# Optimization experiments

Measured on AMD Instinct MI355X. Metric: run time of the kernel, lower is better.

The kernel has to match this reference:

```python
import jax, jax.numpy as jnp
import numpy as np

NUM_EXPERTS = 8
TOP_K = 2
HIDDEN = 2048
INTER = 5632
NUM_TOKENS = 8192


def setup_inputs() -> dict:
    key = jax.random.key(0)
    ks = jax.random.split(key, 5)
    s_h = 1.0 / np.sqrt(HIDDEN)
    s_i = 1.0 / np.sqrt(INTER)
    return {
        "hidden_states": jax.random.normal(ks[0], (NUM_TOKENS, HIDDEN), jnp.float32),
        # router: ReplicatedLinear(hidden, num_experts, bias=False) -> weight [E, H]
        "w_router": jax.random.normal(ks[1], (NUM_EXPERTS, HIDDEN), jnp.float32) * s_h,
        # FusedMoE SiLU-gated MLP per expert: gate/up [E, H, I], down [E, I, H]
        "w_gate": jax.random.normal(ks[2], (NUM_EXPERTS, HIDDEN, INTER), jnp.float32) * s_h,
        "w_up": jax.random.normal(ks[3], (NUM_EXPERTS, HIDDEN, INTER), jnp.float32) * s_h,
        "w_down": jax.random.normal(ks[4], (NUM_EXPERTS, INTER, HIDDEN), jnp.float32) * s_i,
    }


def reference(hidden_states, w_router, w_gate, w_up, w_down):
    x = hidden_states  # [T, H]
    # Router linear (no bias)
    router_logits = x @ w_router.T  # [T, E]
    # FusedMoE topk: softmax over all experts, take top-k, renormalize=False
    probs = jax.nn.softmax(router_logits.astype(jnp.float32), axis=-1)
    topk_w, topk_idx = jax.lax.top_k(probs, TOP_K)  # [T, k]
    topk_w = topk_w.astype(x.dtype)

    out = jnp.zeros_like(x)
    for e in range(NUM_EXPERTS):
        # combine weight for tokens that routed to expert e (0 otherwise)
        w_e = jnp.sum(jnp.where(topk_idx == e, topk_w, 0.0), axis=-1)  # [T]
        h = jax.nn.silu(x @ w_gate[e]) * (x @ w_up[e])  # [T, I]
        out = out + (h @ w_down[e]) * w_e[:, None]
    return out
```

## Files before the change

### kernel.cpp

```cpp
#include <hip/hip_runtime.h>
#include <hip/hip_bf16.h>
#include <cstdint>

#define NTOK 8192
#define NEXP 8
#define HID  2048
#define INTR 5632
#define NT1  44
#define NT2  16

#define TCNT_OFF    4096u
#define SLOT_OFF    65536u
#define T2S_OFF     262144u
#define W2_OFF      393216u
#define LISTS_OFF   524288u
#define WL_OFF      786432u
#define WG_OFF      2097152u
#define WBYTES      184549376u
#define WU_OFF      (WG_OFF + WBYTES)
#define HF_OFF      (WU_OFF + WBYTES)
#define HFBYTES     207618048u
#define XG_OFF      (HF_OFF + HFBYTES)

typedef float f32x4  __attribute__((ext_vector_type(4)));
typedef short s16x8  __attribute__((ext_vector_type(8)));
typedef short s16x4  __attribute__((ext_vector_type(4)));

__device__ __forceinline__ short bfc(float f) {
  __hip_bfloat16 h = __float2bfloat16(f);
  return __builtin_bit_cast(short, h);
}
__device__ __forceinline__ float b2f(short s) {
  unsigned u = ((unsigned)(unsigned short)s) << 16;
  return __builtin_bit_cast(float, u);
}
__device__ __forceinline__ s16x8 pk8(float4 a, float4 b) {
  s16x8 v;
  v[0]=bfc(a.x); v[1]=bfc(a.y); v[2]=bfc(a.z); v[3]=bfc(a.w);
  v[4]=bfc(b.x); v[5]=bfc(b.y); v[6]=bfc(b.z); v[7]=bfc(b.w);
  return v;
}
__device__ __forceinline__ void gload16(const void* g, void* l) {
  __builtin_amdgcn_global_load_lds((const __attribute__((address_space(1))) void*)g,
                                   (__attribute__((address_space(3))) void*)l, 16, 0, 0);
}

#define DSR128(dst, addr, IMM) \
  asm volatile("ds_read_b128 %0, %1 offset:" IMM : "=v"(dst) : "v"(addr))
#define WAITLGKM(N) do { \
  asm volatile("s_waitcnt lgkmcnt(" #N ")" ::: "memory"); \
  __builtin_amdgcn_sched_barrier(0); } while (0)
#define WAITVM(N) do { \
  asm volatile("s_waitcnt vmcnt(" #N ")" ::: "memory"); \
  __builtin_amdgcn_sched_barrier(0); } while (0)

#define MFMA_BF16 __builtin_amdgcn_mfma_f32_16x16x32_bf16

__global__ __launch_bounds__(256, 4) void prep_kernel(
    const float* __restrict__ src, short* __restrict__ dst,
    int KT, int NP, int Nsrc) {
  __shared__ float tile[32 * 132];
  const int b = blockIdx.x;
  const int np = b % NP;
  const int kt = (b / NP) % KT;
  const int e  = b / (NP * KT);
  const int tid = threadIdx.x;
  const float* s = src + (size_t)e * KT * 32 * (size_t)Nsrc + (size_t)kt * 32 * Nsrc + np * 128;
#pragma unroll
  for (int i = 0; i < 4; i++) {
    const int idx = tid + i * 256;
    const int row = idx >> 5, c4 = idx & 31;
    float4 v = *(const float4*)(s + (size_t)row * Nsrc + c4 * 4);
    *(float4*)(tile + row * 132 + c4 * 4) = v;
  }
  __syncthreads();
  short* dbase = dst + ((size_t)(e * KT + kt) * (NP * 8) + np * 8) * 512;
#pragma unroll
  for (int i = 0; i < 2; i++) {
    const int c = tid + i * 256;
    const int lane = c & 63;
    const int nf = c >> 6;
    const int n = nf * 16 + (lane & 15);
    const int kb = (lane >> 4) * 8;
    s16x8 o;
#pragma unroll
    for (int j = 0; j < 8; j++) o[j] = bfc(tile[(kb + j) * 132 + n]);
    *(s16x8*)(dbase + (size_t)c * 8) = o;
  }
}

__global__ void router_kernel(const float* __restrict__ x, const float* __restrict__ wr,
                              int* __restrict__ cnt, int* __restrict__ lists,
                              float* __restrict__ wlists) {
  const int wave = threadIdx.x >> 6;
  const int lane = threadIdx.x & 63;
  const int t = blockIdx.x * 4 + wave;
  if (t >= NTOK) return;
  float acc[NEXP];
#pragma unroll
  for (int e = 0; e < NEXP; e++) acc[e] = 0.f;
  const float* xrow = x + (size_t)t * HID;
#pragma unroll
  for (int j = 0; j < HID / 256; j++) {
    const int k = j * 256 + lane * 4;
    float4 xv = *(const float4*)(xrow + k);
#pragma unroll
    for (int e = 0; e < NEXP; e++) {
      float4 wv = *(const float4*)(wr + e * HID + k);
      acc[e] += xv.x * wv.x + xv.y * wv.y + xv.z * wv.z + xv.w * wv.w;
    }
  }
#pragma unroll
  for (int e = 0; e < NEXP; e++) {
    float v = acc[e];
    for (int off = 32; off; off >>= 1) v += __shfl_xor(v, off, 64);
    acc[e] = v;
  }
  if (lane == 0) {
    float m = acc[0];
#pragma unroll
    for (int e = 1; e < NEXP; e++) m = fmaxf(m, acc[e]);
    float p[NEXP], s = 0.f;
#pragma unroll
    for (int e = 0; e < NEXP; e++) { p[e] = __expf(acc[e] - m); s += p[e]; }
    const float inv = 1.f / s;
    int e1 = 0; float b1 = p[0];
#pragma unroll
    for (int e = 1; e < NEXP; e++) if (p[e] > b1) { b1 = p[e]; e1 = e; }
    int e2 = -1; float b2 = -1.f;
#pragma unroll
    for (int e = 0; e < NEXP; e++) if (e != e1 && p[e] > b2) { b2 = p[e]; e2 = e; }
    const int pos1 = atomicAdd(&cnt[e1], 1);
    lists[e1 * NTOK + pos1] = t; wlists[e1 * NTOK + pos1] = b1 * inv;
    const int pos2 = atomicAdd(&cnt[e2], 1);
    lists[e2 * NTOK + pos2] = t; wlists[e2 * NTOK + pos2] = b2 * inv;
  }
}

__global__ void offsets_kernel(const int* __restrict__ cnt, int* __restrict__ poffs) {
  if (threadIdx.x == 0 && blockIdx.x == 0) {
    int o = 0;
#pragma unroll
    for (int e = 0; e < NEXP; e++) { poffs[e] = o; o += ((cnt[e] + 255) >> 8) << 8; }
    poffs[NEXP] = o;
  }
}

__global__ void slotmap_kernel(const int* __restrict__ cnt, const int* __restrict__ poffs,
                               const int* __restrict__ lists, const float* __restrict__ wlists,
                               int* __restrict__ slotlist, int* __restrict__ tcnt,
                               int* __restrict__ tok2slot, float* __restrict__ w2) {
  const int e = blockIdx.x;
  const int c = cnt[e], base = poffs[e];
  for (int pos = threadIdx.x; pos < c; pos += blockDim.x) {
    const int tok = lists[e * NTOK + pos];
    const int slot = base + pos;
    slotlist[slot] = tok;
    const int j = atomicAdd(&tcnt[tok], 1);
    tok2slot[tok * 2 + j] = slot;
    w2[tok * 2 + j] = wlists[e * NTOK + pos];
  }
}

__global__ __launch_bounds__(256, 4) void gather_kernel(
    const float* __restrict__ x, const int* __restrict__ slotlist,
    short* __restrict__ xg) {
  const int c = blockIdx.x * 256 + threadIdx.x;
  const int cl = c & 63;
  const int fragid = c >> 6;
  const int f = fragid & 15;
  const int kt = (fragid >> 4) & 63;
  const int gmt = fragid >> 10;
  const int tok = slotlist[gmt * 256 + f * 16 + (cl & 15)];
  const float* s = x + (size_t)tok * HID + kt * 32 + (cl >> 4) * 8;
  float4 a = *(const float4*)s, b = *(const float4*)(s + 4);
  *(s16x8*)(xg + (size_t)c * 8) = pk8(a, b);
}

__global__ __launch_bounds__(512, 1) void gemm1_kernel(
    const short* __restrict__ xg, const short* __restrict__ wgb,
    const short* __restrict__ wub, const int* __restrict__ cnt,
    const int* __restrict__ poffs, short* __restrict__ hfrag) {
  const int P = blockIdx.x;
  const int xcd = P & 7, slot = P >> 3;
  const int mt = slot & 31, jj = slot >> 5;
  const int g = jj * 8 + xcd;
  const int e = g / NT1, nt = g % NT1;
  if (mt * 256 >= cnt[e]) return;
  const int gmt = (poffs[e] >> 8) + mt;
  const int tid = threadIdx.x;
  const int w = tid >> 6, lane = tid & 63;
  const int wm = w >> 1, wn = w & 1;

  __shared__ __align__(16) short Lds[3 * 16384];
  const uint32_t ldsbase = (uint32_t)(uintptr_t)&Lds[0];

  const short* srcA  = xg  + (size_t)gmt * 64 * 16 * 512 + tid * 8;
  const short* srcBg = wgb + (((size_t)e * 64) * 352 + nt * 8) * 512 + tid * 8;
  const short* srcBu = wub + (((size_t)e * 64) * 352 + nt * 8) * 512 + tid * 8;

  const uint32_t roA = wm * 4096 + lane * 16;
  const uint32_t roB = 16384 + wn * 4096 + lane * 16;
  const uint32_t roU = 24576 + wn * 4096 + lane * 16;

  f32x4 accG[4][4], accU[4][4];
#pragma unroll
  for (int i = 0; i < 4; i++)
#pragma unroll
    for (int j = 0; j < 4; j++) {
      accG[i][j] = f32x4{0.f, 0.f, 0.f, 0.f};
      accU[i][j] = f32x4{0.f, 0.f, 0.f, 0.f};
    }

#define STG1(WB) do {                                                           \
    short* d = (short*)Lds + ((WB) >> 1);                                       \
    gload16(srcA,          d + w * 512);                                        \
    gload16(srcA + 4096,   d + 4096 + w * 512);                                 \
    gload16(srcBg,         d + 8192 + w * 512);                                 \
    gload16(srcBu,         d + 12288 + w * 512);                                \
    srcA += 8192; srcBg += 180224; srcBu += 180224; } while (0)

#define MMQ(NF)                                                                 \
  { __builtin_amdgcn_s_setprio(1);                                              \
    accG[0][NF] = MFMA_BF16(af[0], bg[NF], accG[0][NF], 0, 0, 0);               \
    accU[0][NF] = MFMA_BF16(af[0], bu[NF], accU[0][NF], 0, 0, 0);               \
    accG[1][NF] = MFMA_BF16(af[1], bg[NF], accG[1][NF], 0, 0, 0);               \
    accU[1][NF] = MFMA_BF16(af[1], bu[NF], accU[1][NF], 0, 0, 0);               \
    accG[2][NF] = MFMA_BF16(af[2], bg[NF], accG[2][NF], 0, 0, 0);               \
    accU[2][NF] = MFMA_BF16(af[2], bu[NF], accU[2][NF], 0, 0, 0);               \
    accG[3][NF] = MFMA_BF16(af[3], bg[NF], accG[3][NF], 0, 0, 0);               \
    accU[3][NF] = MFMA_BF16(af[3], bu[NF], accU[3][NF], 0, 0, 0);               \
    __builtin_amdgcn_s_setprio(0); }

#define G1_BODY(RB, WB, VMN, DOSTG)                                             \
  {                                                                             \
    WAITVM(VMN);                                                                \
    __builtin_amdgcn_s_barrier();                                               \
    const uint32_t rb = ldsbase + (RB);                                         \
    s16x8 af[4], bg[4], bu[4];                                                  \
    DSR128(bg[0], rb + roB, "0");    DSR128(bu[0], rb + roU, "0");              \
    DSR128(af[0], rb + roA, "0");    DSR128(af[1], rb + roA, "1024");           \
    DSR128(af[2], rb + roA, "2048"); DSR128(af[3], rb + roA, "3072");           \
    DSR128(bg[1], rb + roB, "1024"); DSR128(bu[1], rb + roU, "1024");           \
    DSR128(bg[2], rb + roB, "2048"); DSR128(bu[2], rb + roU, "2048");           \
    DSR128(bg[3], rb + roB, "3072"); DSR128(bu[3], rb + roU, "3072");           \
    if (DOSTG) { STG1(WB); }                                                    \
    WAITLGKM(6);                                                                \
    MMQ(0)                                                                      \
    WAITLGKM(4);                                                                \
    MMQ(1)                                                                      \
    WAITLGKM(2);                                                                \
    MMQ(2)                                                                      \
    WAITLGKM(0);                                                                \
    MMQ(3)                                                                      \
  }

  STG1(0);
  STG1(32768);
  for (int it = 0; it < 20; ++it) {
    G1_BODY(0,     65536, 4, 1)
    G1_BODY(32768, 0,     4, 1)
    G1_BODY(65536, 32768, 4, 1)
  }
  G1_BODY(0,     65536, 4, 1)
  G1_BODY(32768, 0,     4, 1)
  G1_BODY(65536, 0,     4, 0)
  G1_BODY(0,     0,     0, 0)
#undef G1_BODY
#undef MMQ
#undef STG1

  short* tr = (short*)Lds;
  __syncthreads();
#pragma unroll
  for (int mf = 0; mf < 4; mf++)
#pragma unroll
    for (int reg = 0; reg < 4; reg++) {
      const int row = wm * 64 + mf * 16 + (lane >> 4) * 4 + reg;
#pragma unroll
      for (int nf = 0; nf < 4; nf++) {
        const int col = wn * 64 + nf * 16 + (lane & 15);
        const float gv = accG[mf][nf][reg];
        const float uv = accU[mf][nf][reg];
        tr[row * 136 + col] = bfc((gv / (1.f + __expf(-gv))) * uv);
      }
    }
  __syncthreads();
  short* hb = hfrag + (((size_t)gmt * 176 + nt * 4) * 16) * 512;
#pragma unroll
  for (int i = 0; i < 8; i++) {
    const int c = tid + i * 512;
    const int cl = c & 63;
    const int f = (c >> 6) & 15;
    const int ktl = c >> 10;
    const int rr = f * 16 + (cl & 15);
    s16x8 v = *(const s16x8*)(tr + rr * 136 + ktl * 32 + (cl >> 4) * 8);
    *(s16x8*)(hb + ((size_t)ktl * 16 + f) * 512 + cl * 8) = v;
  }
}

__global__ __launch_bounds__(512, 4) void gemm2_kernel(
    const short* __restrict__ hfrag, const short* __restrict__ wdb,
    const int* __restrict__ cnt, const int* __restrict__ poffs,
    __hip_bfloat16* __restrict__ pout) {
  const int P = blockIdx.x;
  const int xcd = P & 7, r = P >> 3;
  const int nt = r & 15, emq = r >> 4;
  const int gm = emq * 8 + xcd;
  const int e = gm >> 5, mt = gm & 31;
  if (mt * 256 >= cnt[e]) return;
  const int gmt = (poffs[e] >> 8) + mt;
  const int n0 = nt * 128;
  const int tid = threadIdx.x;
  const int w = tid >> 6, lane = tid & 63;
  const int wm = w >> 1, wn = w & 1;

  __shared__ __align__(16) short Lds[3 * 12288];
  const uint32_t ldsbase = (uint32_t)(uintptr_t)&Lds[0];

  const short* srcA = hfrag + (size_t)gmt * 176 * 16 * 512 + tid * 8;
  const short* srcB = wdb + (((size_t)e * 176) * 128 + nt * 8) * 512 + tid * 8;

  const uint32_t roA = wm * 4096 + lane * 16;
  const uint32_t roB = 16384 + wn * 4096 + lane * 16;

  f32x4 acc[4][4];
#pragma unroll
  for (int i = 0; i < 4; i++)
#pragma unroll
    for (int j = 0; j < 4; j++) acc[i][j] = f32x4{0.f, 0.f, 0.f, 0.f};

#define STG2(WB) do {                                                           \
    short* d = (short*)Lds + ((WB) >> 1);                                       \
    gload16(srcA,        d + w * 512);                                          \
    gload16(srcA + 4096, d + 4096 + w * 512);                                   \
    gload16(srcB,        d + 8192 + w * 512);                                   \
    srcA += 8192; srcB += 65536; } while (0)

#define MMQ2(NF)                                                                \
  { __builtin_amdgcn_s_setprio(1);                                              \
    acc[0][NF] = MFMA_BF16(af[0], bf[NF], acc[0][NF], 0, 0, 0);                 \
    acc[1][NF] = MFMA_BF16(af[1], bf[NF], acc[1][NF], 0, 0, 0);                 \
    acc[2][NF] = MFMA_BF16(af[2], bf[NF], acc[2][NF], 0, 0, 0);                 \
    acc[3][NF] = MFMA_BF16(af[3], bf[NF], acc[3][NF], 0, 0, 0);                 \
    __builtin_amdgcn_s_setprio(0); }

#define G2_BODY(RB, WB, VMN, DOSTG)                                             \
  {                                                                             \
    WAITVM(VMN);                                                                \
    __builtin_amdgcn_s_barrier();                                               \
    const uint32_t rb = ldsbase + (RB);                                         \
    s16x8 af[4], bf[4];                                                         \
    DSR128(bf[0], rb + roB, "0");                                               \
    DSR128(af[0], rb + roA, "0");    DSR128(af[1], rb + roA, "1024");           \
    DSR128(af[2], rb + roA, "2048"); DSR128(af[3], rb + roA, "3072");           \
    DSR128(bf[1], rb + roB, "1024");                                            \
    DSR128(bf[2], rb + roB, "2048");                                            \
    DSR128(bf[3], rb + roB, "3072");                                            \
    if (DOSTG) { STG2(WB); }                                                    \
    WAITLGKM(3);                                                                \
    MMQ2(0)                                                                     \
    WAITLGKM(2);                                                                \
    MMQ2(1)                                                                     \
    WAITLGKM(1);                                                                \
    MMQ2(2)                                                                     \
    WAITLGKM(0);                                                                \
    MMQ2(3)                                                                     \
  }

  STG2(0);
  STG2(24576);
  for (int it = 0; it < 58; ++it) {
    G2_BODY(0,     49152, 3, 1)
    G2_BODY(24576, 0,     3, 1)
    G2_BODY(49152, 24576, 3, 1)
  }
  G2_BODY(0,     0, 3, 0)
  G2_BODY(24576, 0, 0, 0)
#undef G2_BODY
#undef MMQ2
#undef STG2

  const int slotb = poffs[e] + mt * 256;
#pragma unroll
  for (int mf = 0; mf < 4; mf++) {
#pragma unroll
    for (int reg = 0; reg < 4; reg++) {
      const int row = wm * 64 + mf * 16 + (lane >> 4) * 4 + reg;
      __hip_bfloat16* op = pout + (size_t)(slotb + row) * HID + n0 + wn * 64 + (lane & 15);
#pragma unroll
      for (int nf = 0; nf < 4; nf++)
        op[nf * 16] = __float2bfloat16(acc[mf][nf][reg]);
    }
  }
}

__global__ __launch_bounds__(256, 8) void combine_kernel(
    const __hip_bfloat16* __restrict__ pout, const int* __restrict__ tok2slot,
    const float* __restrict__ w2, float* __restrict__ out) {
  const int t = blockIdx.x;
  const int s0 = tok2slot[2 * t], s1 = tok2slot[2 * t + 1];
  const float w0 = w2[2 * t], w1 = w2[2 * t + 1];
  const short* p0 = (const short*)pout + (size_t)s0 * HID;
  const short* p1 = (const short*)pout + (size_t)s1 * HID;
  float* o = out + (size_t)t * HID;
  const int i = threadIdx.x;
  s16x8 a = *(const s16x8*)(p0 + i * 8);
  s16x8 b = *(const s16x8*)(p1 + i * 8);
  float4 r0, r1;
  r0.x = w0 * b2f(a[0]) + w1 * b2f(b[0]);
  r0.y = w0 * b2f(a[1]) + w1 * b2f(b[1]);
  r0.z = w0 * b2f(a[2]) + w1 * b2f(b[2]);
  r0.w = w0 * b2f(a[3]) + w1 * b2f(b[3]);
  r1.x = w0 * b2f(a[4]) + w1 * b2f(b[4]);
  r1.y = w0 * b2f(a[5]) + w1 * b2f(b[5]);
  r1.z = w0 * b2f(a[6]) + w1 * b2f(b[6]);
  r1.w = w0 * b2f(a[7]) + w1 * b2f(b[7]);
  *(float4*)(o + i * 8) = r0;
  *(float4*)(o + i * 8 + 4) = r1;
}

extern "C" void kernel_launch(void* const* d_in, const int* in_sizes, int n_in,
                              void* d_out, int out_size, void* d_ws, size_t ws_size,
                              hipStream_t stream) {
  const float* x  = (const float*)d_in[0];
  const float* wr = (const float*)d_in[1];
  const float* wg = (const float*)d_in[2];
  const float* wu = (const float*)d_in[3];
  const float* wd = (const float*)d_in[4];
  float* out = (float*)d_out;
  char* ws = (char*)d_ws;

  int* cnt      = (int*)ws;
  int* poffs    = (int*)(ws + 64);
  int* tcnt     = (int*)(ws + TCNT_OFF);
  int* slotlist = (int*)(ws + SLOT_OFF);
  int* tok2slot = (int*)(ws + T2S_OFF);
  float* w2     = (float*)(ws + W2_OFF);
  int* lists    = (int*)(ws + LISTS_OFF);
  float* wlists = (float*)(ws + WL_OFF);
  short* wgb    = (short*)(ws + WG_OFF);
  short* wub    = (short*)(ws + WU_OFF);
  short* wdb    = (short*)(ws + WG_OFF);
  short* hfrag  = (short*)(ws + HF_OFF);
  short* xg     = (short*)(ws + XG_OFF);
  __hip_bfloat16* pout = (__hip_bfloat16*)(ws + XG_OFF);

  hipMemsetAsync(ws, 0, 256, stream);
  hipMemsetAsync(ws + TCNT_OFF, 0, 32768, stream);
  hipMemsetAsync(ws + SLOT_OFF, 0, 73728, stream);

  router_kernel<<<NTOK / 4, 256, 0, stream>>>(x, wr, cnt, lists, wlists);
  offsets_kernel<<<1, 64, 0, stream>>>(cnt, poffs);
  slotmap_kernel<<<NEXP, 256, 0, stream>>>(cnt, poffs, lists, wlists, slotlist, tcnt, tok2slot, w2);
  gather_kernel<<<18432, 256, 0, stream>>>(x, slotlist, xg);
  prep_kernel<<<NEXP * 64 * 44, 256, 0, stream>>>(wg, wgb, 64, 44, INTR);
  prep_kernel<<<NEXP * 64 * 44, 256, 0, stream>>>(wu, wub, 64, 44, INTR);
  gemm1_kernel<<<8 * 32 * NT1, 512, 0, stream>>>(xg, wgb, wub, cnt, poffs, hfrag);
  prep_kernel<<<NEXP * 176 * 16, 256, 0, stream>>>(wd, wdb, 176, 16, HID);
  gemm2_kernel<<<8 * 16 * 32, 512, 0, stream>>>(hfrag, wdb, cnt, poffs, pout);
  combine_kernel<<<NTOK, 256, 0, stream>>>(pout, tok2slot, w2, out);
}
```

Measured before the change: 1.670 ms.

## Load gemm1 A fragments straight to registers and double-buffer B through LDS

In gemm1, the A (token) fragments are now loaded from global memory directly into registers with inline global_load_dwordx4, and no longer staged through LDS. The gate and up weight tiles are loaded into registers and written to LDS with ds_write into two buffers instead of three. This cuts LDS use to about 68KB so two 512-thread blocks can share a CU (launch bounds raised to 2), and it removes the LDS reads for A. The cost is more register pressure from holding two sets of A fragments plus prefetched B. The hand-tuned waitcnt counts and buffer alternation must be exactly right to avoid races. The gemm2 change only renames arrays to scalars.

```diff
diff --git a/kernel.cpp b/kernel.cpp
--- a/kernel.cpp
+++ b/kernel.cpp
@@ -47,12 +47,25 @@
 
 #define DSR128(dst, addr, IMM) \
   asm volatile("ds_read_b128 %0, %1 offset:" IMM : "=v"(dst) : "v"(addr))
+#define DSW128(addr, data, IMM) \
+  asm volatile("ds_write_b128 %0, %1 offset:" IMM :: "v"(addr), "v"(data))
 #define WAITLGKM(N) do { \
   asm volatile("s_waitcnt lgkmcnt(" #N ")" ::: "memory"); \
   __builtin_amdgcn_sched_barrier(0); } while (0)
 #define WAITVM(N) do { \
   asm volatile("s_waitcnt vmcnt(" #N ")" ::: "memory"); \
   __builtin_amdgcn_sched_barrier(0); } while (0)
+
+#define LOADA4(D0, D1, D2, D3, PTR) \
+  asm volatile("global_load_dwordx4 %0, %4, off\n\t" \
+               "global_load_dwordx4 %1, %4, off offset:1024\n\t" \
+               "global_load_dwordx4 %2, %4, off offset:2048\n\t" \
+               "global_load_dwordx4 %3, %4, off offset:3072" \
+               : "=&v"(D0), "=&v"(D1), "=&v"(D2), "=&v"(D3) : "v"(PTR))
+#define LOADB2(DG, DU, PG, PU) \
+  asm volatile("global_load_dwordx4 %0, %2, off\n\t" \
+               "global_load_dwordx4 %1, %3, off" \
+               : "=&v"(DG), "=&v"(DU) : "v"(PG), "v"(PU))
 
 #define MFMA_BF16 __builtin_amdgcn_mfma_f32_16x16x32_bf16
 
@@ -177,7 +190,7 @@
   *(s16x8*)(xg + (size_t)c * 8) = pk8(a, b);
 }
 
-__global__ __launch_bounds__(512, 1) void gemm1_kernel(
+__global__ __launch_bounds__(512, 2) void gemm1_kernel(
     const short* __restrict__ xg, const short* __restrict__ wgb,
     const short* __restrict__ wub, const int* __restrict__ cnt,
     const int* __restrict__ poffs, short* __restrict__ hfrag) {
@@ -192,16 +205,16 @@
   const int w = tid >> 6, lane = tid & 63;
   const int wm = w >> 1, wn = w & 1;
 
-  __shared__ __align__(16) short Lds[3 * 16384];
+  __shared__ __align__(16) short Lds[34816];
   const uint32_t ldsbase = (uint32_t)(uintptr_t)&Lds[0];
 
-  const short* srcA  = xg  + (size_t)gmt * 64 * 16 * 512 + tid * 8;
+  const short* srcA  = xg + (size_t)gmt * 64 * 16 * 512 + (size_t)(wm * 4) * 512 + lane * 8;
   const short* srcBg = wgb + (((size_t)e * 64) * 352 + nt * 8) * 512 + tid * 8;
   const short* srcBu = wub + (((size_t)e * 64) * 352 + nt * 8) * 512 + tid * 8;
 
-  const uint32_t roA = wm * 4096 + lane * 16;
-  const uint32_t roB = 16384 + wn * 4096 + lane * 16;
-  const uint32_t roU = 24576 + wn * 4096 + lane * 16;
+  const uint32_t roB = wn * 4096 + lane * 16;
+  const uint32_t roU = 8192 + wn * 4096 + lane * 16;
+  const uint32_t awr = ldsbase + tid * 16;
 
   f32x4 accG[4][4], accU[4][4];
 #pragma unroll
@@ -212,63 +225,71 @@
       accU[i][j] = f32x4{0.f, 0.f, 0.f, 0.f};
     }
 
-#define STG1(WB) do {                                                           \
-    short* d = (short*)Lds + ((WB) >> 1);                                       \
-    gload16(srcA,          d + w * 512);                                        \
-    gload16(srcA + 4096,   d + 4096 + w * 512);                                 \
-    gload16(srcBg,         d + 8192 + w * 512);                                 \
-    gload16(srcBu,         d + 12288 + w * 512);                                \
-    srcA += 8192; srcBg += 180224; srcBu += 180224; } while (0)
-
-#define MMQ(NF)                                                                 \
+  s16x8 arA0, arA1, arA2, arA3, arB0, arB1, arB2, arB3;
+  s16x8 g0p, u0p, g1p, u1p;
+
+  LOADB2(g0p, u0p, srcBg, srcBu); srcBg += 180224; srcBu += 180224;
+  LOADA4(arA0, arA1, arA2, arA3, srcA); srcA += 8192;
+  LOADB2(g1p, u1p, srcBg, srcBu); srcBg += 180224; srcBu += 180224;
+  WAITVM(6);
+  DSW128(awr, g0p, "0");
+  DSW128(awr, u0p, "8192");
+  WAITLGKM(0);
+
+#define MMQ(NF, BG, BU, A0, A1, A2, A3)                                         \
   { __builtin_amdgcn_s_setprio(1);                                              \
-    accG[0][NF] = MFMA_BF16(af[0], bg[NF], accG[0][NF], 0, 0, 0);               \
-    accU[0][NF] = MFMA_BF16(af[0], bu[NF], accU[0][NF], 0, 0, 0);               \
-    accG[1][NF] = MFMA_BF16(af[1], bg[NF], accG[1][NF], 0, 0, 0);               \
-    accU[1][NF] = MFMA_BF16(af[1], bu[NF], accU[1][NF], 0, 0, 0);               \
-    accG[2][NF] = MFMA_BF16(af[2], bg[NF], accG[2][NF], 0, 0, 0);               \
-    accU[2][NF] = MFMA_BF16(af[2], bu[NF], accU[2][NF], 0, 0, 0);               \
-    accG[3][NF] = MFMA_BF16(af[3], bg[NF], accG[3][NF], 0, 0, 0);               \
-    accU[3][NF] = MFMA_BF16(af[3], bu[NF], accU[3][NF], 0, 0, 0);               \
+    accG[0][NF] = MFMA_BF16(A0, BG, accG[0][NF], 0, 0, 0);                      \
+    accU[0][NF] = MFMA_BF16(A0, BU, accU[0][NF], 0, 0, 0);                      \
+    accG[1][NF] = MFMA_BF16(A1, BG, accG[1][NF], 0, 0, 0);                      \
+    accU[1][NF] = MFMA_BF16(A1, BU, accU[1][NF], 0, 0, 0);                      \
+    accG[2][NF] = MFMA_BF16(A2, BG, accG[2][NF], 0, 0, 0);                      \
+    accU[2][NF] = MFMA_BF16(A2, BU, accU[2][NF], 0, 0, 0);                      \
+    accG[3][NF] = MFMA_BF16(A3, BG, accG[3][NF], 0, 0, 0);                      \
+    accU[3][NF] = MFMA_BF16(A3, BU, accU[3][NF], 0, 0, 0);                      \
     __builtin_amdgcn_s_setprio(0); }
 
-#define G1_BODY(RB, WB, VMN, DOSTG)                                             \
+#define G1_BODY(RBOFF, WIG, WIU, U0,U1,U2,U3, L0,L1,L2,L3, WPG,WPU, LPG,LPU,    \
+                VTOP, DO_A, DO_WR, DO_LB, LGA, LGB, LGC, LGD)                   \
   {                                                                             \
-    WAITVM(VMN);                                                                \
-    __builtin_amdgcn_s_barrier();                                               \
-    const uint32_t rb = ldsbase + (RB);                                         \
-    s16x8 af[4], bg[4], bu[4];                                                  \
-    DSR128(bg[0], rb + roB, "0");    DSR128(bu[0], rb + roU, "0");              \
-    DSR128(af[0], rb + roA, "0");    DSR128(af[1], rb + roA, "1024");           \
-    DSR128(af[2], rb + roA, "2048"); DSR128(af[3], rb + roA, "3072");           \
-    DSR128(bg[1], rb + roB, "1024"); DSR128(bu[1], rb + roU, "1024");           \
-    DSR128(bg[2], rb + roB, "2048"); DSR128(bu[2], rb + roU, "2048");           \
-    DSR128(bg[3], rb + roB, "3072"); DSR128(bu[3], rb + roU, "3072");           \
-    if (DOSTG) { STG1(WB); }                                                    \
-    WAITLGKM(6);                                                                \
-    MMQ(0)                                                                      \
-    WAITLGKM(4);                                                                \
-    MMQ(1)                                                                      \
-    WAITLGKM(2);                                                                \
-    MMQ(2)                                                                      \
-    WAITLGKM(0);                                                                \
-    MMQ(3)                                                                      \
-  }
-
-  STG1(0);
-  STG1(32768);
-  for (int it = 0; it < 20; ++it) {
-    G1_BODY(0,     65536, 4, 1)
-    G1_BODY(32768, 0,     4, 1)
-    G1_BODY(65536, 32768, 4, 1)
-  }
-  G1_BODY(0,     65536, 4, 1)
-  G1_BODY(32768, 0,     4, 1)
-  G1_BODY(65536, 0,     4, 0)
-  G1_BODY(0,     0,     0, 0)
+    WAITVM(VTOP);                                       \
+    __builtin_amdgcn_s_barrier();                     \
+    const uint32_t rb = ldsbase + (RBOFF);                                      \
+    s16x8 bg0, bg1, bg2, bg3, bu0, bu1, bu2, bu3;                               \
+    DSR128(bg0, rb + roB, "0");    DSR128(bu0, rb + roU, "0");                  \
+    DSR128(bg1, rb + roB, "1024"); DSR128(bu1, rb + roU, "1024");               \
+    DSR128(bg2, rb + roB, "2048"); DSR128(bu2, rb + roU, "2048");               \
+    DSR128(bg3, rb + roB, "3072"); DSR128(bu3, rb + roU, "3072");               \
+    if (DO_A) { LOADA4(L0, L1, L2, L3, srcA); srcA += 8192; }                   \
+    if (DO_WR) {                                                                \
+      WAITVM(4);                                     \
+      DSW128(awr, WPG, WIG);                                                    \
+      DSW128(awr, WPU, WIU);                                                    \
+    }                                                                           \
+    if (DO_LB) { LOADB2(LPG, LPU, srcBg, srcBu);                                \
+                 srcBg += 180224; srcBu += 180224; }                            \
+    WAITLGKM(LGA);                                                              \
+    MMQ(0, bg0, bu0, U0, U1, U2, U3)                                            \
+    WAITLGKM(LGB);                                                              \
+    MMQ(1, bg1, bu1, U0, U1, U2, U3)                                            \
+    WAITLGKM(LGC);                                                              \
+    MMQ(2, bg2, bu2, U0, U1, U2, U3)                                            \
+    WAITLGKM(LGD);                                                              \
+    MMQ(3, bg3, bu3, U0, U1, U2, U3)                                            \
+    WAITLGKM(0);                         \
+  }
+
+  for (int it = 0; it < 31; ++it) {
+    G1_BODY(0,     "16384","24576", arA0,arA1,arA2,arA3, arB0,arB1,arB2,arB3,
+            g1p,u1p, g0p,u0p, 2, 1, 1, 1, 8, 6, 4, 2)
+    G1_BODY(16384, "0","8192",      arB0,arB1,arB2,arB3, arA0,arA1,arA2,arA3,
+            g0p,u0p, g1p,u1p, 2, 1, 1, 1, 8, 6, 4, 2)
+  }
+  G1_BODY(0,     "16384","24576", arA0,arA1,arA2,arA3, arB0,arB1,arB2,arB3,
+          g1p,u1p, g0p,u0p, 2, 1, 1, 0, 8, 6, 4, 2)
+  G1_BODY(16384, "0","8192",      arB0,arB1,arB2,arB3, arA0,arA1,arA2,arA3,
+          g0p,u0p, g1p,u1p, 0, 0, 0, 0, 6, 4, 2, 0)
 #undef G1_BODY
 #undef MMQ
-#undef STG1
 
   short* tr = (short*)Lds;
   __syncthreads();
@@ -337,12 +358,12 @@
     gload16(srcB,        d + 8192 + w * 512);                                   \
     srcA += 8192; srcB += 65536; } while (0)
 
-#define MMQ2(NF)                                                                \
+#define MMQ2(NF, BF)                                                            \
   { __builtin_amdgcn_s_setprio(1);                                              \
-    acc[0][NF] = MFMA_BF16(af[0], bf[NF], acc[0][NF], 0, 0, 0);                 \
-    acc[1][NF] = MFMA_BF16(af[1], bf[NF], acc[1][NF], 0, 0, 0);                 \
-    acc[2][NF] = MFMA_BF16(af[2], bf[NF], acc[2][NF], 0, 0, 0);                 \
-    acc[3][NF] = MFMA_BF16(af[3], bf[NF], acc[3][NF], 0, 0, 0);                 \
+    acc[0][NF] = MFMA_BF16(af0, BF, acc[0][NF], 0, 0, 0);                       \
+    acc[1][NF] = MFMA_BF16(af1, BF, acc[1][NF], 0, 0, 0);                       \
+    acc[2][NF] = MFMA_BF16(af2, BF, acc[2][NF], 0, 0, 0);                       \
+    acc[3][NF] = MFMA_BF16(af3, BF, acc[3][NF], 0, 0, 0);                       \
     __builtin_amdgcn_s_setprio(0); }
 
 #define G2_BODY(RB, WB, VMN, DOSTG)                                             \
@@ -350,22 +371,22 @@
     WAITVM(VMN);                                                                \
     __builtin_amdgcn_s_barrier();                                               \
     const uint32_t rb = ldsbase + (RB);                                         \
-    s16x8 af[4], bf[4];                                                         \
-    DSR128(bf[0], rb + roB, "0");                                               \
-    DSR128(af[0], rb + roA, "0");    DSR128(af[1], rb + roA, "1024");           \
-    DSR128(af[2], rb + roA, "2048"); DSR128(af[3], rb + roA, "3072");           \
-    DSR128(bf[1], rb + roB, "1024");                                            \
-    DSR128(bf[2], rb + roB, "2048");                                            \
-    DSR128(bf[3], rb + roB, "3072");                                            \
+    s16x8 af0, af1, af2, af3, bf0, bf1, bf2, bf3;                               \
+    DSR128(bf0, rb + roB, "0");                                                 \
+    DSR128(af0, rb + roA, "0");    DSR128(af1, rb + roA, "1024");               \
+    DSR128(af2, rb + roA, "2048"); DSR128(af3, rb + roA, "3072");               \
+    DSR128(bf1, rb + roB, "1024");                                              \
+    DSR128(bf2, rb + roB, "2048");                                              \
+    DSR128(bf3, rb + roB, "3072");                                              \
     if (DOSTG) { STG2(WB); }                                                    \
     WAITLGKM(3);                                                                \
-    MMQ2(0)                                                                     \
+    MMQ2(0, bf0)                                                                \
     WAITLGKM(2);                                                                \
-    MMQ2(1)                                                                     \
+    MMQ2(1, bf1)                                                                \
     WAITLGKM(1);                                                                \
-    MMQ2(2)                                                                     \
+    MMQ2(2, bf2)                                                                \
     WAITLGKM(0);                                                                \
-    MMQ2(3)                                                                     \
+    MMQ2(3, bf3)                                                                \
   }
 
   STG2(0);
```

Measured after the change: 1.780 ms. 1.07x slower.
